# Optimization experiments

Hardware: AMD Instinct MI355X
Metric: run time of the kernel (lower is better)

The kernel has to match this reference:

```python
import jax, jax.numpy as jnp
import numpy as np
from jax import lax

SCORE_THRESH = 0.05
NMS_THRESH = 0.5
DETECTIONS_PER_IMG = 100
MIN_SIZE = 0.01
AREA_THRESH = 0.0
BOX_W = (10.0, 10.0, 5.0, 5.0)
BBOX_XFORM_CLIP = float(np.log(1000.0 / 16.0))


def setup_inputs() -> dict:
    key = jax.random.key(0)
    B, N, C = 8, 4000, 91
    H, W = 800, 1333
    k1, k2, k3 = jax.random.split(key, 3)
    # scale logits so a realistic fraction of softmax scores exceed score_thresh
    class_logits = jax.random.normal(k1, (B * N, C), jnp.float32) * 2.0
    box_regression = jax.random.normal(k2, (B * N, C * 4), jnp.float32)
    u = jax.random.uniform(k3, (B, N, 4), jnp.float32)
    x1 = u[..., 0] * (W - 50)
    y1 = u[..., 1] * (H - 50)
    bw = u[..., 2] * 200.0 + 4.0
    bh = u[..., 3] * 200.0 + 4.0
    proposals = jnp.stack([x1, y1, jnp.minimum(x1 + bw, W), jnp.minimum(y1 + bh, H)], axis=-1)
    return {"class_logits": class_logits, "box_regression": box_regression,
            "proposals": proposals, "image_h": H, "image_w": W}


def _decode(rel, props):
    # torchvision BoxCoder.decode: props [P,4], rel [P, C*4] -> [P, C, 4]
    w = props[:, 2] - props[:, 0]
    h = props[:, 3] - props[:, 1]
    cx = props[:, 0] + 0.5 * w
    cy = props[:, 1] + 0.5 * h
    rel = rel.reshape(rel.shape[0], -1, 4)
    dx = rel[..., 0] / BOX_W[0]
    dy = rel[..., 1] / BOX_W[1]
    dw = jnp.minimum(rel[..., 2] / BOX_W[2], BBOX_XFORM_CLIP)
    dh = jnp.minimum(rel[..., 3] / BOX_W[3], BBOX_XFORM_CLIP)
    pcx = dx * w[:, None] + cx[:, None]
    pcy = dy * h[:, None] + cy[:, None]
    pw = jnp.exp(dw) * w[:, None]
    ph = jnp.exp(dh) * h[:, None]
    return jnp.stack([pcx - 0.5 * pw, pcy - 0.5 * ph, pcx + 0.5 * pw, pcy + 0.5 * ph], axis=-1)


def _nms_image(boxes, scores, labels_f, valid, off_unit):
    # greedy batched NMS (class-offset trick) producing first DETECTIONS_PER_IMG survivors
    NEG = -1e9
    s0 = jnp.where(valid, scores, NEG)
    ob = boxes + (labels_f * off_unit)[:, None]  # per-class coordinate offset
    areas = (ob[:, 2] - ob[:, 0]) * (ob[:, 3] - ob[:, 1])

    def step(s, _):
        i = jnp.argmax(s)
        sc = s[i]
        ok = sc > (NEG / 2)
        obi = ob[i]
        ix1 = jnp.maximum(obi[0], ob[:, 0])
        iy1 = jnp.maximum(obi[1], ob[:, 1])
        ix2 = jnp.minimum(obi[2], ob[:, 2])
        iy2 = jnp.minimum(obi[3], ob[:, 3])
        inter = jnp.maximum(ix2 - ix1, 0.0) * jnp.maximum(iy2 - iy1, 0.0)
        ai = (obi[2] - obi[0]) * (obi[3] - obi[1])
        iou = inter / jnp.maximum(ai + areas - inter, 1e-9)
        sup = (iou > NMS_THRESH) & ok
        s = jnp.where(sup, NEG, s).at[i].set(NEG)
        return s, (i, jnp.where(ok, sc, 0.0), ok)

    _, (idx, out_sc, ok) = lax.scan(step, s0, None, length=DETECTIONS_PER_IMG)
    out_boxes = boxes[idx] * ok[:, None]
    out_labels = jnp.where(ok, labels_f[idx], 0.0)
    areas_out = (out_boxes[:, 2] - out_boxes[:, 0]) * (out_boxes[:, 3] - out_boxes[:, 1])
    keep = ok & (areas_out >= AREA_THRESH)
    return out_boxes * keep[:, None], out_sc * keep, jnp.where(keep, out_labels, 0.0), keep


def reference(class_logits, box_regression, proposals, image_h, image_w):
    B, N, _ = proposals.shape
    C = class_logits.shape[-1]
    pred_boxes = _decode(box_regression, proposals.reshape(B * N, 4)).reshape(B, N, C, 4)
    pred_scores = jax.nn.softmax(class_logits, axis=-1).reshape(B, N, C)
    # clip boxes to image
    x = jnp.clip(pred_boxes[..., 0::2], 0.0, float(image_w))
    y = jnp.clip(pred_boxes[..., 1::2], 0.0, float(image_h))
    pred_boxes = jnp.stack([x[..., 0], y[..., 0], x[..., 1], y[..., 1]], axis=-1)
    # drop background class 0, flatten (proposal, class) pairs
    M = N * (C - 1)
    boxes = pred_boxes[:, :, 1:, :].reshape(B, M, 4)
    scores = pred_scores[:, :, 1:].reshape(B, M)
    labels_f = jnp.broadcast_to(jnp.arange(1, C, dtype=boxes.dtype)[None, :], (N, C - 1)).reshape(M)
    ws = boxes[..., 2] - boxes[..., 0]
    hs = boxes[..., 3] - boxes[..., 1]
    valid = (scores > SCORE_THRESH) & (ws >= MIN_SIZE) & (hs >= MIN_SIZE)
    off_unit = float(max(image_h, image_w)) + 1.0
    out_boxes, out_scores, out_labels_f, keep = jax.vmap(
        lambda b, s, v: _nms_image(b, s, labels_f, v, off_unit))(boxes, scores, valid)
    return out_boxes, out_scores, out_labels_f.astype(jnp.int32), keep
```

## Files before the change

### kernel.cpp

```cpp
#include <hip/hip_runtime.h>
#include <stdint.h>

typedef uint32_t u32;
typedef unsigned long long u64;

#define NB 8
#define NPER 4000
#define NC 91
#define NCLS 90
#define NDET 100
#define CHUNKS 64
#define RPB 63
#define LBIN 16
#define CCAP 63
#define BINCAP 512
#define SURVCAP 9216
#define NSFIX (NCLS * NDET)
#define FKCAP 1024
#define VPT 36
#define NBIN 1152
#define SLO 0x3D4CCCCEu
#define SSH 15

__device__ __forceinline__ float4 decode_clip(float4 rel, float w, float h,
                                              float cx, float cy, float W, float H) {
  const float XCLIP = 4.135166556742356f;
  float dx = rel.x / 10.0f;
  float dy = rel.y / 10.0f;
  float dw = fminf(rel.z / 5.0f, XCLIP);
  float dh = fminf(rel.w / 5.0f, XCLIP);
  float qcx = dx * w + cx;
  float qcy = dy * h + cy;
  float qw = expf(dw) * w;
  float qh = expf(dh) * h;
  float x1 = qcx - 0.5f * qw, y1 = qcy - 0.5f * qh;
  float x2 = qcx + 0.5f * qw, y2 = qcy + 0.5f * qh;
  x1 = fminf(fmaxf(x1, 0.0f), W);
  x2 = fminf(fmaxf(x2, 0.0f), W);
  y1 = fminf(fmaxf(y1, 0.0f), H);
  y2 = fminf(fmaxf(y2, 0.0f), H);
  return make_float4(x1, y1, x2, y2);
}

__device__ __forceinline__ float rdlane(float v, int sl) {
  return __int_as_float(__builtin_amdgcn_readlane(__float_as_int(v), sl));
}

__device__ __forceinline__ void emit_row(int r, int rl, int lane, float sA, float sB,
    float W, float H, const float4* __restrict__ props4, const float4* __restrict__ breg4,
    u32* s_cnt, u64 (*s_key)[LBIN], float4 (*s_box)[LBIN],
    size_t chbase, u64* __restrict__ bins_key, float4* __restrict__ bins_box) {
  bool eA_ok = (lane >= 1) && (sA > 0.05f);
  bool eB_ok = (lane < NC - 64) && (sB > 0.05f);
  if (!(eA_ok || eB_ok)) return;
  float4 p = props4[r];
  float w = p.z - p.x, h = p.w - p.y;
  float cx = p.x + 0.5f * w, cy = p.y + 0.5f * h;
  if (eA_ok) {
    float4 raw = decode_clip(breg4[(size_t)r * NC + lane], w, h, cx, cy, W, H);
    if (((raw.z - raw.x) >= 0.01f) && ((raw.w - raw.y) >= 0.01f)) {
      int ci = lane - 1;
      u32 orig = (u32)(rl * NCLS + ci);
      u64 key = ((u64)__float_as_uint(sA) << 22) | (u64)(0x3FFFFFu - orig);
      u32 lp = atomicAdd(&s_cnt[ci], 1u);
      if (lp < LBIN) { s_key[ci][lp] = key; s_box[ci][lp] = raw; }
      else if (lp < CCAP) {
        size_t o = (chbase + ci) * CCAP + lp;
        bins_key[o] = key; bins_box[o] = raw;
      }
    }
  }
  if (eB_ok) {
    float4 raw = decode_clip(breg4[(size_t)r * NC + 64 + lane], w, h, cx, cy, W, H);
    if (((raw.z - raw.x) >= 0.01f) && ((raw.w - raw.y) >= 0.01f)) {
      int ci = 63 + lane;
      u32 orig = (u32)(rl * NCLS + ci);
      u64 key = ((u64)__float_as_uint(sB) << 22) | (u64)(0x3FFFFFu - orig);
      u32 lp = atomicAdd(&s_cnt[ci], 1u);
      if (lp < LBIN) { s_key[ci][lp] = key; s_box[ci][lp] = raw; }
      else if (lp < CCAP) {
        size_t o = (chbase + ci) * CCAP + lp;
        bins_key[o] = key; bins_box[o] = raw;
      }
    }
  }
}

__global__ __launch_bounds__(1024) void k_score(const float* __restrict__ logits,
    const float* __restrict__ boxreg, const float* __restrict__ props,
    const int* __restrict__ dh, const int* __restrict__ dw,
    u32* cnt_g, u64* bins_key, float4* bins_box) {
  __shared__ u64 s_key[NCLS][LBIN];
  __shared__ float4 s_box[NCLS][LBIN];
  __shared__ u32 s_cnt[NCLS];
  int tid = threadIdx.x;
  int b = blockIdx.x / CHUNKS;
  int chunk = blockIdx.x % CHUNKS;
  int wave = tid >> 6, lane = tid & 63;
  if (tid < NCLS) s_cnt[tid] = 0u;
  __syncthreads();

  float H = (float)dh[0], W = (float)dw[0];
  const float4* props4 = (const float4*)props;
  const float4* breg4 = (const float4*)boxreg;
  size_t chbase = ((size_t)(b * CHUNKS + chunk)) * NCLS;

  for (int rloc = wave; rloc < RPB; rloc += 32) {
    int rloc1 = rloc + 16;
    int rl0 = chunk * RPB + rloc;
    int rl1 = chunk * RPB + rloc1;
    bool v0 = (rl0 < NPER);
    bool v1 = (rloc1 < RPB) && (rl1 < NPER);
    int r0 = b * NPER + (v0 ? rl0 : 0);
    int r1 = b * NPER + (v1 ? rl1 : 0);
    const float* l0 = logits + (size_t)r0 * NC;
    const float* l1 = logits + (size_t)r1 * NC;
    float xA0 = l0[lane];
    float xA1 = l1[lane];
    float xB0 = (lane < NC - 64) ? l0[64 + lane] : -3.0e38f;
    float xB1 = (lane < NC - 64) ? l1[64 + lane] : -3.0e38f;
    float mx0 = fmaxf(xA0, xB0);
    float mx1 = fmaxf(xA1, xB1);
    for (int o = 32; o; o >>= 1) {
      mx0 = fmaxf(mx0, __shfl_xor(mx0, o));
      mx1 = fmaxf(mx1, __shfl_xor(mx1, o));
    }
    float eA0 = expf(xA0 - mx0);
    float eA1 = expf(xA1 - mx1);
    float eB0 = (lane < NC - 64) ? expf(xB0 - mx0) : 0.0f;
    float eB1 = (lane < NC - 64) ? expf(xB1 - mx1) : 0.0f;
    float sm0 = eA0 + eB0;
    float sm1 = eA1 + eB1;
    for (int o = 32; o; o >>= 1) {
      sm0 += __shfl_xor(sm0, o);
      sm1 += __shfl_xor(sm1, o);
    }
    if (v0) emit_row(r0, rl0, lane, eA0 / sm0, eB0 / sm0, W, H, props4, breg4,
                     s_cnt, s_key, s_box, chbase, bins_key, bins_box);
    if (v1) emit_row(r1, rl1, lane, eA1 / sm1, eB1 / sm1, W, H, props4, breg4,
                     s_cnt, s_key, s_box, chbase, bins_key, bins_box);
  }
  __syncthreads();
  if (tid < NCLS) cnt_g[chbase + tid] = s_cnt[tid];
  for (int idx = tid; idx < NCLS * LBIN; idx += 1024) {
    int ci = idx / LBIN, j = idx % LBIN;
    if ((u32)j < s_cnt[ci]) {
      size_t o = (chbase + ci) * CCAP + (u32)j;
      bins_key[o] = s_key[ci][j];
      bins_box[o] = s_box[ci][j];
    }
  }
}

__global__ __launch_bounds__(256) void k_nms_class(const u32* __restrict__ cnt_g,
    const u64* __restrict__ bins_key, const float4* __restrict__ bins_box,
    u64* skey, float4* sbox, const int* __restrict__ dh, const int* __restrict__ dw) {
  __shared__ u64 k[BINCAP];
  __shared__ float4 boxu[BINCAP];
  __shared__ u64 ks[BINCAP];
  __shared__ float4 boxs[BINCAP];
  __shared__ float4 s_sb[NDET];
  __shared__ float s_sa[NDET];
  __shared__ u64 s_sk[NDET];
  __shared__ u32 s_sid[NDET];
  __shared__ u32 s_off[64];
  __shared__ u32 s_c[64];
  __shared__ u32 s_n;

  int b = blockIdx.x / NCLS;
  int ci = blockIdx.x % NCLS;
  int tid = threadIdx.x;
  u64* outk = skey + (size_t)b * SURVCAP + (size_t)ci * NDET;
  float4* outb = sbox + (size_t)b * SURVCAP + (size_t)ci * NDET;

  if (tid < 64) {
    u32 c = cnt_g[((size_t)(b * CHUNKS + tid)) * NCLS + ci];
    if (c > CCAP) c = CCAP;
    s_c[tid] = c;
    u32 inc = c;
    for (int o = 1; o < 64; o <<= 1) {
      u32 v = __shfl_up(inc, o);
      if (tid >= o) inc += v;
    }
    s_off[tid] = inc - c;
    if (tid == 63) s_n = (inc > BINCAP) ? BINCAP : inc;
  }
  __syncthreads();
  int n = (int)s_n;
  if (n <= 0) {
    for (int i = tid; i < NDET; i += 256) outk[i] = 0ull;
    return;
  }
  {
    int chunk = tid & 63, start = tid >> 6;
    u32 cc = s_c[chunk], of = s_off[chunk];
    size_t src = (((size_t)(b * CHUNKS + chunk)) * NCLS + ci) * CCAP;
    for (u32 i = (u32)start; i < cc; i += 4) {
      u32 d = of + i;
      if (d < (u32)BINCAP) { k[d] = bins_key[src + i]; boxu[d] = bins_box[src + i]; }
    }
  }
  __syncthreads();
  for (int i = tid; i < n; i += 256) {
    u64 ki = k[i];
    u32 rank = 0;
    int j = 0;
    for (; j + 4 <= n; j += 4) {
      rank += (k[j] > ki) ? 1u : 0u;
      rank += (k[j + 1] > ki) ? 1u : 0u;
      rank += (k[j + 2] > ki) ? 1u : 0u;
      rank += (k[j + 3] > ki) ? 1u : 0u;
    }
    for (; j < n; ++j) rank += (k[j] > ki) ? 1u : 0u;
    ks[rank] = ki;
    boxs[rank] = boxu[i];
  }
  __syncthreads();
  if (tid >= 64) return;

  float H = (float)dh[0], W = (float)dw[0];
  float loff = (fmaxf(H, W) + 1.0f) * (float)(ci + 1);
  int lane = tid;
  int S = 0;
  for (int base = 0; base < n && S < NDET; base += 64) {
    int i = base + lane;
    bool have = (i < n);
    u64 mykey = 0ull;
    float4 Bb = make_float4(0.f, 0.f, 0.f, 0.f);
    float aB = 0.f;
    if (have) {
      mykey = ks[i];
      float4 raw = boxs[i];
      Bb = make_float4(raw.x + loff, raw.y + loff, raw.z + loff, raw.w + loff);
      aB = (Bb.z - Bb.x) * (Bb.w - Bb.y);
    }
    bool alive = have;
    for (int s = 0; s < S; ++s) {
      float4 A = s_sb[s];
      float aA = s_sa[s];
      float ix1 = fmaxf(A.x, Bb.x), iy1 = fmaxf(A.y, Bb.y);
      float ix2 = fminf(A.z, Bb.z), iy2 = fminf(A.w, Bb.w);
      float inter = fmaxf(ix2 - ix1, 0.0f) * fmaxf(iy2 - iy1, 0.0f);
      float iou = inter / fmaxf(aA + aB - inter, 1e-9f);
      if (alive && iou > 0.5f) alive = false;
    }
    u64 mask = __ballot(alive);
    while (mask && S < NDET) {
      int j = __builtin_ctzll(mask);
      int js = __builtin_amdgcn_readfirstlane(j);
      float Ax = rdlane(Bb.x, js), Ay = rdlane(Bb.y, js);
      float Az = rdlane(Bb.z, js), Aw = rdlane(Bb.w, js);
      float aA = rdlane(aB, js);
      if (lane == js) {
        s_sb[S] = Bb; s_sa[S] = aB; s_sk[S] = mykey; s_sid[S] = (u32)i;
      }
      float ix1 = fmaxf(Ax, Bb.x), iy1 = fmaxf(Ay, Bb.y);
      float ix2 = fminf(Az, Bb.z), iy2 = fminf(Aw, Bb.w);
      float inter = fmaxf(ix2 - ix1, 0.0f) * fmaxf(iy2 - iy1, 0.0f);
      float iou = inter / fmaxf(aA + aB - inter, 1e-9f);
      if (alive && iou > 0.5f) alive = false;
      ++S;
      mask = __ballot(alive);
    }
  }
  for (int i2 = lane; i2 < NDET; i2 += 64) {
    if (i2 < S) {
      outk[i2] = s_sk[i2];
      outb[i2] = boxs[s_sid[i2]];
    } else {
      outk[i2] = 0ull;
    }
  }
}

__global__ __launch_bounds__(256) void k_top(const u64* __restrict__ skey,
    const float4* __restrict__ sbox, float* out) {
  __shared__ u32 hist[NBIN];
  __shared__ u64 fk[FKCAP];
  __shared__ u32 fs[FKCAP];
  __shared__ u64 okey[NDET];
  __shared__ u32 osrc[NDET];
  __shared__ u32 s_cnt[2];
  __shared__ u32 s_bin;

  int b = blockIdx.x;
  int tid = threadIdx.x;
  const u64* kb = skey + (size_t)b * SURVCAP;

  u32 sc[VPT];
#pragma unroll
  for (int v = 0; v < VPT; ++v) {
    u32 j = (u32)tid + (u32)v * 256u;
    sc[v] = (j < NSFIX) ? (u32)(kb[j] >> 22) : 0u;
  }
  for (int i = tid; i < NBIN; i += 256) hist[i] = 0u;
  if (tid == 0) { s_cnt[0] = 0; s_cnt[1] = 0; }
  __syncthreads();

#pragma unroll
  for (int v = 0; v < VPT; ++v) {
    u32 s = sc[v];
    if (s > SLO) atomicAdd(&hist[(s - SLO) >> SSH], 1u);
  }
  __syncthreads();

  if (tid < 64) {
    int lane = tid;
    int base = lane * (NBIN / 64);
    u32 csum = 0;
#pragma unroll
    for (int kk2 = 0; kk2 < NBIN / 64; ++kk2) csum += hist[base + kk2];
    u32 suf = csum;
    for (int o = 1; o < 64; o <<= 1) {
      u32 v = __shfl_down(suf, o);
      if (lane + o < 64) suf += v;
    }
    u64 m = __ballot(suf >= NDET);
    int B = 0;
    if (m) {
      int c = 63 - __builtin_clzll(m);
      u32 rest = (c < 63) ? (u32)__shfl((int)suf, c + 1) : 0u;
      u32 acc = rest;
      int cb = c * (NBIN / 64);
      for (int kk2 = (NBIN / 64) - 1; kk2 >= 0; --kk2) {
        acc += hist[cb + kk2];
        if (acc >= NDET) { B = cb + kk2; break; }
      }
    }
    if (lane == 0) s_bin = (u32)B;
  }
  __syncthreads();
  u32 B = s_bin;

#pragma unroll
  for (int v = 0; v < VPT; ++v) {
    u32 s = sc[v];
    if (s > SLO && ((s - SLO) >> SSH) > B) {
      u32 j = (u32)tid + (u32)v * 256u;
      u32 p = atomicAdd(&s_cnt[0], 1u);
      if (p < FKCAP) { fk[p] = kb[j]; fs[p] = j; }
    }
  }
  __syncthreads();
  if (tid == 0) s_cnt[1] = s_cnt[0];
  __syncthreads();
#pragma unroll
  for (int v = 0; v < VPT; ++v) {
    u32 s = sc[v];
    if (s > SLO && ((s - SLO) >> SSH) == B) {
      u32 j = (u32)tid + (u32)v * 256u;
      u32 p = atomicAdd(&s_cnt[1], 1u);
      if (p < FKCAP) { fk[p] = kb[j]; fs[p] = j; }
    }
  }
  __syncthreads();
  u32 tot = s_cnt[1];
  if (tot > FKCAP) tot = FKCAP;
  if (tid >= 64) return;

  for (int i = tid; i < NDET; i += 64) okey[i] = 0ull;
  for (int i = tid; i < (int)tot; i += 64) {
    u64 ki = fk[i];
    u32 rank = 0;
    for (int j = 0; j < (int)tot; ++j) rank += (fk[j] > ki) ? 1u : 0u;
    if (rank < NDET) { okey[rank] = ki; osrc[rank] = fs[i]; }
  }
  for (int i = tid; i < NDET; i += 64) {
    u64 key = okey[i];
    float b0 = 0.f, b1 = 0.f, b2 = 0.f, b3 = 0.f, sc2 = 0.f, lb = 0.f, kp = 0.f;
    if (key) {
      float4 bx = sbox[(size_t)b * SURVCAP + osrc[i]];
      b0 = bx.x; b1 = bx.y; b2 = bx.z; b3 = bx.w;
      sc2 = __uint_as_float((u32)(key >> 22));
      u32 orig = 0x3FFFFFu - (u32)(key & 0x3FFFFFu);
      lb = (float)(orig % NCLS + 1u);
      kp = 1.0f;
    }
    float* ob = out + ((size_t)b * NDET + i) * 4;
    ob[0] = b0; ob[1] = b1; ob[2] = b2; ob[3] = b3;
    out[NB * NDET * 4 + b * NDET + i] = sc2;
    out[NB * NDET * 5 + b * NDET + i] = lb;
    out[NB * NDET * 6 + b * NDET + i] = kp;
  }
}

extern "C" void kernel_launch(void* const* d_in, const int* in_sizes, int n_in,
                              void* d_out, int out_size, void* d_ws, size_t ws_size,
                              hipStream_t stream) {
  const float* logits = (const float*)d_in[0];
  const float* boxreg = (const float*)d_in[1];
  const float* props  = (const float*)d_in[2];
  const int* dh = (const int*)d_in[3];
  const int* dw = (const int*)d_in[4];
  float* out = (float*)d_out;

  char* ws = (char*)d_ws;
  u32* cnt_g = (u32*)ws;
  char* p0 = ws + (((size_t)NB * CHUNKS * NCLS * 4 + 255) & ~(size_t)255);
  u64* bins_key = (u64*)p0;
  char* p1 = p0 + (size_t)NB * CHUNKS * NCLS * CCAP * 8;
  float4* bins_box = (float4*)p1;
  char* p2 = p1 + (size_t)NB * CHUNKS * NCLS * CCAP * 16;
  u64* skey = (u64*)p2;
  float4* sbox = (float4*)(p2 + (size_t)NB * SURVCAP * 8);
  (void)ws_size;

  k_score<<<NB * CHUNKS, 1024, 0, stream>>>(logits, boxreg, props, dh, dw,
                                            cnt_g, bins_key, bins_box);
  k_nms_class<<<NB * NCLS, 256, 0, stream>>>(cnt_g, bins_key, bins_box,
                                             skey, sbox, dh, dw);
  k_top<<<NB, 256, 0, stream>>>(skey, sbox, out);
}
```

Measured before the change: 159.2 us.

## Halve score block size and select two NMS survivors per ballot iteration

The scoring kernel now runs 512 threads per block, and each of its 8 waves handles 8 rows through a fixed 4-iteration loop with pairs spaced 32 apart. Before, 16 waves each handled up to 4 rows. In the per-class NMS kernel the serial survivor loop now takes the first two alive candidates at once: it checks whether the second survives the first, then suppresses the rest against both. This is meant to halve the number of ballot round-trips. It adds extra readlane traffic and branching per iteration, and the smaller score block may lower parallelism per chunk.

```diff
diff --git a/kernel.cpp b/kernel.cpp
--- a/kernel.cpp
+++ b/kernel.cpp
@@ -86,7 +86,7 @@
   }
 }
 
-__global__ __launch_bounds__(1024) void k_score(const float* __restrict__ logits,
+__global__ __launch_bounds__(512) void k_score(const float* __restrict__ logits,
     const float* __restrict__ boxreg, const float* __restrict__ props,
     const int* __restrict__ dh, const int* __restrict__ dw,
     u32* cnt_g, u64* bins_key, float4* bins_box) {
@@ -105,8 +105,9 @@
   const float4* breg4 = (const float4*)boxreg;
   size_t chbase = ((size_t)(b * CHUNKS + chunk)) * NCLS;
 
-  for (int rloc = wave; rloc < RPB; rloc += 32) {
-    int rloc1 = rloc + 16;
+  for (int it = 0; it < 4; ++it) {
+    int rloc = wave + (it << 3);
+    int rloc1 = rloc + 32;
     int rl0 = chunk * RPB + rloc;
     int rl1 = chunk * RPB + rloc1;
     bool v0 = (rl0 < NPER);
@@ -142,7 +143,7 @@
   }
   __syncthreads();
   if (tid < NCLS) cnt_g[chbase + tid] = s_cnt[tid];
-  for (int idx = tid; idx < NCLS * LBIN; idx += 1024) {
+  for (int idx = tid; idx < NCLS * LBIN; idx += 512) {
     int ci = idx / LBIN, j = idx % LBIN;
     if ((u32)j < s_cnt[ci]) {
       size_t o = (chbase + ci) * CCAP + (u32)j;
@@ -246,20 +247,49 @@
     }
     u64 mask = __ballot(alive);
     while (mask && S < NDET) {
-      int j = __builtin_ctzll(mask);
-      int js = __builtin_amdgcn_readfirstlane(j);
-      float Ax = rdlane(Bb.x, js), Ay = rdlane(Bb.y, js);
-      float Az = rdlane(Bb.z, js), Aw = rdlane(Bb.w, js);
-      float aA = rdlane(aB, js);
-      if (lane == js) {
+      int j0 = __builtin_amdgcn_readfirstlane(__builtin_ctzll(mask));
+      float A0x = rdlane(Bb.x, j0), A0y = rdlane(Bb.y, j0);
+      float A0z = rdlane(Bb.z, j0), A0w = rdlane(Bb.w, j0);
+      float a0 = rdlane(aB, j0);
+      u64 m2 = mask & (mask - 1);
+      bool have1 = (m2 != 0ull) && (S + 1 < NDET);
+      int j1 = 0;
+      float A1x = 0.f, A1y = 0.f, A1z = 0.f, A1w = 0.f, a1 = 0.f;
+      if (have1) {
+        j1 = __builtin_amdgcn_readfirstlane(__builtin_ctzll(m2));
+        A1x = rdlane(Bb.x, j1); A1y = rdlane(Bb.y, j1);
+        A1z = rdlane(Bb.z, j1); A1w = rdlane(Bb.w, j1);
+        a1 = rdlane(aB, j1);
+      }
+      float ix1 = fmaxf(A0x, Bb.x), iy1 = fmaxf(A0y, Bb.y);
+      float ix2 = fminf(A0z, Bb.z), iy2 = fminf(A0w, Bb.w);
+      float inter = fmaxf(ix2 - ix1, 0.0f) * fmaxf(iy2 - iy1, 0.0f);
+      float iou0 = inter / fmaxf(a0 + aB - inter, 1e-9f);
+      bool sel1 = false;
+      if (have1) {
+        float jx1 = fmaxf(A0x, A1x), jy1 = fmaxf(A0y, A1y);
+        float jx2 = fminf(A0z, A1z), jy2 = fminf(A0w, A1w);
+        float jint = fmaxf(jx2 - jx1, 0.0f) * fmaxf(jy2 - jy1, 0.0f);
+        float iou01 = jint / fmaxf(a0 + a1 - jint, 1e-9f);
+        sel1 = !(iou01 > 0.5f);
+      }
+      if (lane == j0) {
         s_sb[S] = Bb; s_sa[S] = aB; s_sk[S] = mykey; s_sid[S] = (u32)i;
       }
-      float ix1 = fmaxf(Ax, Bb.x), iy1 = fmaxf(Ay, Bb.y);
-      float ix2 = fminf(Az, Bb.z), iy2 = fminf(Aw, Bb.w);
-      float inter = fmaxf(ix2 - ix1, 0.0f) * fmaxf(iy2 - iy1, 0.0f);
-      float iou = inter / fmaxf(aA + aB - inter, 1e-9f);
-      if (alive && iou > 0.5f) alive = false;
-      ++S;
+      if (alive && iou0 > 0.5f) alive = false;
+      if (sel1) {
+        if (lane == j1) {
+          s_sb[S + 1] = Bb; s_sa[S + 1] = aB; s_sk[S + 1] = mykey; s_sid[S + 1] = (u32)i;
+        }
+        float kx1 = fmaxf(A1x, Bb.x), ky1 = fmaxf(A1y, Bb.y);
+        float kx2 = fminf(A1z, Bb.z), ky2 = fminf(A1w, Bb.w);
+        float kint = fmaxf(kx2 - kx1, 0.0f) * fmaxf(ky2 - ky1, 0.0f);
+        float iou1 = kint / fmaxf(a1 + aB - kint, 1e-9f);
+        if (alive && iou1 > 0.5f) alive = false;
+        S += 2;
+      } else {
+        S += 1;
+      }
       mask = __ballot(alive);
     }
   }
@@ -405,8 +435,8 @@
   float4* sbox = (float4*)(p2 + (size_t)NB * SURVCAP * 8);
   (void)ws_size;
 
-  k_score<<<NB * CHUNKS, 1024, 0, stream>>>(logits, boxreg, props, dh, dw,
-                                            cnt_g, bins_key, bins_box);
+  k_score<<<NB * CHUNKS, 512, 0, stream>>>(logits, boxreg, props, dh, dw,
+                                           cnt_g, bins_key, bins_box);
   k_nms_class<<<NB * NCLS, 256, 0, stream>>>(cnt_g, bins_key, bins_box,
                                              skey, sbox, dh, dw);
   k_top<<<NB, 256, 0, stream>>>(skey, sbox, out);
```

Measured after the change: 165.3 us. 3.9% more time.
